# Performance work log

Hardware: AMD Instinct MI355X
Metric: run time of the kernel (lower is better)

## Reference

```python
import jax, jax.numpy as jnp
import numpy as np

N, D, OUT, K = 100000, 256, 128, 10
N1, B = 40960, 4096


def setup_inputs() -> dict:
    key = jax.random.key(0)
    k1, k2, k3, k4, k5, k6, k7 = jax.random.split(key, 7)
    raw_features = jax.random.normal(k1, (N, D), dtype=jnp.float32)
    # xavier-ish init for SageLayer weights [out, 2*in]
    W1 = jax.random.normal(k2, (OUT, 2 * D), dtype=jnp.float32) * (2.0 / (OUT + 2 * D)) ** 0.5
    W2 = jax.random.normal(k3, (OUT, 2 * OUT), dtype=jnp.float32) * (2.0 / (OUT + 2 * OUT)) ** 0.5
    nodes1 = jax.random.randint(k4, (N1,), 0, N)              # layer-1 node ids into raw table
    neighs1 = jax.random.randint(k5, (N1, K), 0, N)           # sampled neighbors (ids into raw table)
    map2 = jax.random.randint(k6, (B,), 0, N1)                # self-index of batch nodes into layer-1 rows
    neighs2 = jax.random.randint(k7, (B, K), 0, N1)           # sampled neighbors (rows of layer-1 embs)
    return {"raw_features": raw_features, "W1": W1, "W2": W2,
            "nodes1": nodes1, "neighs1": neighs1, "map2": map2, "neighs2": neighs2}


def reference(raw_features, W1, W2, nodes1, neighs1, map2, neighs2):
    # Layer 1: mean-aggregate sampled neighbor features (= mask.div(num_neigh).mm(embed_matrix))
    agg1 = jnp.mean(raw_features[neighs1], axis=1)                      # [N1, D]
    self1 = raw_features[nodes1]                                        # [N1, D]
    h1 = jax.nn.relu(jnp.concatenate([self1, agg1], axis=1) @ W1.T)     # [N1, OUT]
    # Layer 2
    agg2 = jnp.mean(h1[neighs2], axis=1)                                # [B, OUT]
    self2 = h1[map2]                                                    # [B, OUT]
    h2 = jax.nn.relu(jnp.concatenate([self2, agg2], axis=1) @ W2.T)     # [B, OUT]
    return h2
```

## Files before the change

### kernel.cpp

```cpp
#include <hip/hip_runtime.h>
#include <hip/hip_bf16.h>

#define N_RAW  100000
#define DIM    256
#define OUTD   128
#define KN     10
#define N1N    40960
#define BATCH  4096

typedef __attribute__((ext_vector_type(8))) short bf16x8;
typedef __attribute__((ext_vector_type(4))) float f32x4;
typedef unsigned int u32;

static __device__ inline float b2f(short s) {
  unsigned u = ((unsigned)(unsigned short)s) << 16;
  return __builtin_bit_cast(float, u);
}
static __device__ inline short f2b(float f) {
  unsigned u = __builtin_bit_cast(unsigned, f);
  unsigned r = (u + 0x7fff + ((u >> 16) & 1)) >> 16;
  return (short)r;
}

static __device__ inline void gload_lds16(const void* g, void* l) {
  __builtin_amdgcn_global_load_lds((const __attribute__((address_space(1))) u32*)g,
                                   (__attribute__((address_space(3))) u32*)l, 16, 0, 0);
}

__global__ void build_wc(const float* __restrict__ W1, const float* __restrict__ W2,
                         short* __restrict__ W1c, short* __restrict__ W2c) {
  int i = blockIdx.x * blockDim.x + threadIdx.x;
  {
    int j = i >> 8, k = i & 255;
    float v = (j < OUTD) ? W1[j * (2 * DIM) + k] : W1[(j - OUTD) * (2 * DIM) + DIM + k];
    u32 byte = (u32)(j * 512 + k * 2) ^ ((u32)(j & 7) << 4);
    *(short*)((char*)W1c + byte) = f2b(v);
  }
  if (i < 256 * 128) {
    int j = i >> 7, k = i & 127;
    float v = (j < OUTD) ? W2[j * (2 * OUTD) + k] : W2[(j - OUTD) * (2 * OUTD) + OUTD + k];
    u32 byte = (u32)(j * 256 + k * 2) ^ ((u32)(j & 7) << 4);
    *(short*)((char*)W2c + byte) = f2b(v);
  }
}

__launch_bounds__(512, 2)
__global__ void gemm_P(const float* __restrict__ raw, const short* __restrict__ W1c,
                       short* __restrict__ P) {
  __shared__ short Wlds[256 * 256];
  const int tid  = threadIdx.x;
  const int wave = tid >> 6, lane = tid & 63;
  const int r16  = lane & 15, kg = lane >> 4;
  const int m0   = blockIdx.x * 128 + wave * 16;

  int arow = m0 + r16; if (arow >= N_RAW) arow = N_RAW - 1;
  const float* xrow = raw + (size_t)arow * DIM + kg * 8;
  float4 af[16];
#pragma unroll
  for (int ks = 0; ks < 8; ++ks) {
    af[2 * ks]     = *(const float4*)(xrow + ks * 32);
    af[2 * ks + 1] = *(const float4*)(xrow + ks * 32 + 4);
  }

#pragma unroll
  for (int it = 0; it < 16; ++it)
    gload_lds16((const char*)W1c + it * 8192 + tid * 16,
                (char*)Wlds + it * 8192 + wave * 1024);
  __syncthreads();

  bf16x8 ab[8];
#pragma unroll
  for (int ks = 0; ks < 8; ++ks) {
    bf16x8 t;
    t[0] = f2b(af[2 * ks].x);     t[1] = f2b(af[2 * ks].y);
    t[2] = f2b(af[2 * ks].z);     t[3] = f2b(af[2 * ks].w);
    t[4] = f2b(af[2 * ks + 1].x); t[5] = f2b(af[2 * ks + 1].y);
    t[6] = f2b(af[2 * ks + 1].z); t[7] = f2b(af[2 * ks + 1].w);
    ab[ks] = t;
  }

  f32x4 acc[16];
#pragma unroll
  for (int n = 0; n < 16; ++n) acc[n] = (f32x4){0.f, 0.f, 0.f, 0.f};

#pragma unroll
  for (int ks = 0; ks < 8; ++ks) {
#pragma unroll
    for (int n = 0; n < 16; ++n) {
      u32 byte = (u32)((n * 16 + r16) * 512 + ks * 64 + kg * 16) ^ ((u32)(r16 & 7) << 4);
      bf16x8 b = *(const bf16x8*)((const char*)Wlds + byte);
      acc[n] = __builtin_amdgcn_mfma_f32_16x16x32_bf16(ab[ks], b, acc[n], 0, 0, 0);
    }
  }

#pragma unroll
  for (int n = 0; n < 16; ++n)
#pragma unroll
    for (int j = 0; j < 4; ++j) {
      int r = m0 + kg * 4 + j;
      if (r < N_RAW) P[(size_t)r * 256 + (n * 16 + r16)] = f2b(acc[n][j]);
    }
}

__launch_bounds__(512, 4)
__global__ void gemm_Q(const short* __restrict__ h1, const short* __restrict__ W2c,
                       short* __restrict__ Q) {
  __shared__ short Wlds[256 * 128];
  const int tid  = threadIdx.x;
  const int wave = tid >> 6, lane = tid & 63;
  const int r16  = lane & 15, kg = lane >> 4;
  const int m0   = blockIdx.x * 128 + wave * 16;

  const short* xrow = h1 + (size_t)(m0 + r16) * OUTD + kg * 8;
  bf16x8 ab[4];
#pragma unroll
  for (int ks = 0; ks < 4; ++ks) ab[ks] = *(const bf16x8*)(xrow + ks * 32);

#pragma unroll
  for (int it = 0; it < 8; ++it)
    gload_lds16((const char*)W2c + it * 8192 + tid * 16,
                (char*)Wlds + it * 8192 + wave * 1024);
  __syncthreads();

  f32x4 acc[16];
#pragma unroll
  for (int n = 0; n < 16; ++n) acc[n] = (f32x4){0.f, 0.f, 0.f, 0.f};

#pragma unroll
  for (int ks = 0; ks < 4; ++ks) {
#pragma unroll
    for (int n = 0; n < 16; ++n) {
      u32 byte = (u32)((n * 16 + r16) * 256 + ks * 64 + kg * 16) ^ ((u32)(r16 & 7) << 4);
      bf16x8 b = *(const bf16x8*)((const char*)Wlds + byte);
      acc[n] = __builtin_amdgcn_mfma_f32_16x16x32_bf16(ab[ks], b, acc[n], 0, 0, 0);
    }
  }

#pragma unroll
  for (int n = 0; n < 16; ++n)
#pragma unroll
    for (int j = 0; j < 4; ++j)
      Q[(size_t)(m0 + kg * 4 + j) * 256 + (n * 16 + r16)] = f2b(acc[n][j]);
}

__global__ void gather1(const short* __restrict__ P, const int* __restrict__ nodes1,
                        const int* __restrict__ neighs1, short* __restrict__ h1) {
  int g = threadIdx.x >> 4, t = threadIdx.x & 15;
  int row = blockIdx.x * 16 + g;
  int sn = nodes1[row];
  bf16x8 sv = *(const bf16x8*)(P + (size_t)sn * 256 + t * 8);
  float acc[8];
#pragma unroll
  for (int e = 0; e < 8; ++e) acc[e] = 0.f;
#pragma unroll
  for (int k = 0; k < KN; ++k) {
    int nn = neighs1[row * KN + k];
    bf16x8 nv = *(const bf16x8*)(P + (size_t)nn * 256 + 128 + t * 8);
#pragma unroll
    for (int e = 0; e < 8; ++e) acc[e] += b2f(nv[e]);
  }
  bf16x8 o;
#pragma unroll
  for (int e = 0; e < 8; ++e) o[e] = f2b(fmaxf(b2f(sv[e]) + 0.1f * acc[e], 0.f));
  *(bf16x8*)(h1 + (size_t)row * OUTD + t * 8) = o;
}

__global__ void gather2(const short* __restrict__ Q, const int* __restrict__ map2,
                        const int* __restrict__ neighs2, float* __restrict__ out) {
  int g = threadIdx.x >> 4, t = threadIdx.x & 15;
  int row = blockIdx.x * 16 + g;
  int sn = map2[row];
  bf16x8 sv = *(const bf16x8*)(Q + (size_t)sn * 256 + t * 8);
  float acc[8];
#pragma unroll
  for (int e = 0; e < 8; ++e) acc[e] = 0.f;
#pragma unroll
  for (int k = 0; k < KN; ++k) {
    int nn = neighs2[row * KN + k];
    bf16x8 nv = *(const bf16x8*)(Q + (size_t)nn * 256 + 128 + t * 8);
#pragma unroll
    for (int e = 0; e < 8; ++e) acc[e] += b2f(nv[e]);
  }
  float* orow = out + (size_t)row * OUTD + t * 8;
  float4 o0, o1;
  o0.x = fmaxf(b2f(sv[0]) + 0.1f * acc[0], 0.f);
  o0.y = fmaxf(b2f(sv[1]) + 0.1f * acc[1], 0.f);
  o0.z = fmaxf(b2f(sv[2]) + 0.1f * acc[2], 0.f);
  o0.w = fmaxf(b2f(sv[3]) + 0.1f * acc[3], 0.f);
  o1.x = fmaxf(b2f(sv[4]) + 0.1f * acc[4], 0.f);
  o1.y = fmaxf(b2f(sv[5]) + 0.1f * acc[5], 0.f);
  o1.z = fmaxf(b2f(sv[6]) + 0.1f * acc[6], 0.f);
  o1.w = fmaxf(b2f(sv[7]) + 0.1f * acc[7], 0.f);
  *(float4*)orow = o0;
  *(float4*)(orow + 4) = o1;
}

extern "C" void kernel_launch(void* const* d_in, const int* in_sizes, int n_in,
                              void* d_out, int out_size, void* d_ws, size_t ws_size,
                              hipStream_t stream) {
  const float* raw     = (const float*)d_in[0];
  const float* W1      = (const float*)d_in[1];
  const float* W2      = (const float*)d_in[2];
  const int*   nodes1  = (const int*)d_in[3];
  const int*   neighs1 = (const int*)d_in[4];
  const int*   map2    = (const int*)d_in[5];
  const int*   neighs2 = (const int*)d_in[6];
  float* out = (float*)d_out;

  char* ws = (char*)d_ws;
  short* W1c = (short*)(ws);
  short* W2c = (short*)(ws + 131072);
  short* P   = (short*)(ws + 196608);
  short* Q   = (short*)(ws + 196608);
  short* h1  = (short*)(ws + 51396608);

  build_wc<<<256, 256, 0, stream>>>(W1, W2, W1c, W2c);
  gemm_P<<<782, 512, 0, stream>>>(raw, W1c, P);
  gather1<<<N1N / 16, 256, 0, stream>>>(P, nodes1, neighs1, h1);
  gemm_Q<<<N1N / 128, 512, 0, stream>>>(h1, W2c, Q);
  gather2<<<BATCH / 16, 256, 0, stream>>>(Q, map2, neighs2, out);
}
```

Before: 93.22 us.

## Split GEMMs across output-column quarters to shrink LDS and raise occupancy

```diff
diff --git a/kernel.cpp b/kernel.cpp
--- a/kernel.cpp
+++ b/kernel.cpp
@@ -7,9 +7,12 @@
 #define KN     10
 #define N1N    40960
 #define BATCH  4096
+#define SNP    6250
+#define SNQ    2560
 
 typedef __attribute__((ext_vector_type(8))) short bf16x8;
 typedef __attribute__((ext_vector_type(4))) float f32x4;
+typedef __attribute__((ext_vector_type(4))) unsigned int u32x4;
 typedef unsigned int u32;
 
 static __device__ inline float b2f(short s) {
@@ -21,7 +24,11 @@
   unsigned r = (u + 0x7fff + ((u >> 16) & 1)) >> 16;
   return (short)r;
 }
-
+static __device__ inline u32 cvtpk(float lo, float hi) {
+  u32 r;
+  asm("v_cvt_pk_bf16_f32 %0, %1, %2" : "=v"(r) : "v"(lo), "v"(hi));
+  return r;
+}
 static __device__ inline void gload_lds16(const void* g, void* l) {
   __builtin_amdgcn_global_load_lds((const __attribute__((address_space(1))) u32*)g,
                                    (__attribute__((address_space(3))) u32*)l, 16, 0, 0);
@@ -33,114 +40,127 @@
   {
     int j = i >> 8, k = i & 255;
     float v = (j < OUTD) ? W1[j * (2 * DIM) + k] : W1[(j - OUTD) * (2 * DIM) + DIM + k];
-    u32 byte = (u32)(j * 512 + k * 2) ^ ((u32)(j & 7) << 4);
+    u32 byte = (u32)((j >> 6) * 32768 + (k >> 6) * 8192 + (j & 63) * 128)
+             + (((u32)(2 * (k & 63))) ^ ((u32)(j & 7) << 4));
     *(short*)((char*)W1c + byte) = f2b(v);
   }
   if (i < 256 * 128) {
     int j = i >> 7, k = i & 127;
     float v = (j < OUTD) ? W2[j * (2 * OUTD) + k] : W2[(j - OUTD) * (2 * OUTD) + OUTD + k];
-    u32 byte = (u32)(j * 256 + k * 2) ^ ((u32)(j & 7) << 4);
+    u32 byte = (u32)((j >> 6) * 16384 + (k >> 6) * 8192 + (j & 63) * 128)
+             + (((u32)(2 * (k & 63))) ^ ((u32)(j & 7) << 4));
     *(short*)((char*)W2c + byte) = f2b(v);
   }
 }
 
-__launch_bounds__(512, 2)
-__global__ void gemm_P(const float* __restrict__ raw, const short* __restrict__ W1c,
-                       short* __restrict__ P) {
-  __shared__ short Wlds[256 * 256];
+__global__ __launch_bounds__(512, 8)
+void gemm_P(const float* __restrict__ raw, const short* __restrict__ W1c,
+            short* __restrict__ P) {
+  __shared__ char Blds[32768];
   const int tid  = threadIdx.x;
   const int wave = tid >> 6, lane = tid & 63;
   const int r16  = lane & 15, kg = lane >> 4;
-  const int m0   = blockIdx.x * 128 + wave * 16;
-
-  int arow = m0 + r16; if (arow >= N_RAW) arow = N_RAW - 1;
-  const float* xrow = raw + (size_t)arow * DIM + kg * 8;
-  float4 af[16];
-#pragma unroll
-  for (int ks = 0; ks < 8; ++ks) {
-    af[2 * ks]     = *(const float4*)(xrow + ks * 32);
-    af[2 * ks + 1] = *(const float4*)(xrow + ks * 32 + 4);
-  }
-
-#pragma unroll
-  for (int it = 0; it < 16; ++it)
-    gload_lds16((const char*)W1c + it * 8192 + tid * 16,
-                (char*)Wlds + it * 8192 + wave * 1024);
+  const int q    = blockIdx.x & 3;
+  const int sg   = blockIdx.x >> 2;
+  const u32 swz  = (u32)(r16 & 7) << 4;
+
+#pragma unroll
+  for (int it = 0; it < 4; ++it)
+    gload_lds16((const char*)W1c + q * 32768 + it * 8192 + wave * 1024 + lane * 16,
+                Blds + it * 8192 + wave * 1024);
   __syncthreads();
 
-  bf16x8 ab[8];
-#pragma unroll
-  for (int ks = 0; ks < 8; ++ks) {
-    bf16x8 t;
-    t[0] = f2b(af[2 * ks].x);     t[1] = f2b(af[2 * ks].y);
-    t[2] = f2b(af[2 * ks].z);     t[3] = f2b(af[2 * ks].w);
-    t[4] = f2b(af[2 * ks + 1].x); t[5] = f2b(af[2 * ks + 1].y);
-    t[6] = f2b(af[2 * ks + 1].z); t[7] = f2b(af[2 * ks + 1].w);
-    ab[ks] = t;
-  }
-
-  f32x4 acc[16];
-#pragma unroll
-  for (int n = 0; n < 16; ++n) acc[n] = (f32x4){0.f, 0.f, 0.f, 0.f};
-
-#pragma unroll
-  for (int ks = 0; ks < 8; ++ks) {
-#pragma unroll
-    for (int n = 0; n < 16; ++n) {
-      u32 byte = (u32)((n * 16 + r16) * 512 + ks * 64 + kg * 16) ^ ((u32)(r16 & 7) << 4);
-      bf16x8 b = *(const bf16x8*)((const char*)Wlds + byte);
-      acc[n] = __builtin_amdgcn_mfma_f32_16x16x32_bf16(ab[ks], b, acc[n], 0, 0, 0);
+  const int s = sg * 8 + wave;
+  if (s >= SNP) return;
+
+  const float* x = raw + (size_t)(s * 16 + r16) * DIM + kg * 8;
+
+  f32x4 acc[4];
+#pragma unroll
+  for (int n = 0; n < 4; ++n) acc[n] = (f32x4){0.f, 0.f, 0.f, 0.f};
+
+#pragma unroll
+  for (int p = 0; p < 4; ++p) {
+    f32x4 v0 = *(const f32x4*)(x + p * 64);
+    f32x4 v1 = *(const f32x4*)(x + p * 64 + 4);
+    f32x4 v2 = *(const f32x4*)(x + p * 64 + 32);
+    f32x4 v3 = *(const f32x4*)(x + p * 64 + 36);
+
+    u32x4 t0, t1;
+    t0[0] = cvtpk(v0[0], v0[1]); t0[1] = cvtpk(v0[2], v0[3]);
+    t0[2] = cvtpk(v1[0], v1[1]); t0[3] = cvtpk(v1[2], v1[3]);
+    t1[0] = cvtpk(v2[0], v2[1]); t1[1] = cvtpk(v2[2], v2[3]);
+    t1[2] = cvtpk(v3[0], v3[1]); t1[3] = cvtpk(v3[2], v3[3]);
+    bf16x8 ab0 = __builtin_bit_cast(bf16x8, t0);
+    bf16x8 ab1 = __builtin_bit_cast(bf16x8, t1);
+
+#pragma unroll
+    for (int n = 0; n < 4; ++n) {
+      u32 base = (u32)(p * 8192 + (n * 16 + r16) * 128);
+      bf16x8 b0 = *(const bf16x8*)(Blds + base + (((u32)(kg * 16)) ^ swz));
+      bf16x8 b1 = *(const bf16x8*)(Blds + base + (((u32)(64 + kg * 16)) ^ swz));
+      acc[n] = __builtin_amdgcn_mfma_f32_16x16x32_bf16(ab0, b0, acc[n], 0, 0, 0);
+      acc[n] = __builtin_amdgcn_mfma_f32_16x16x32_bf16(ab1, b1, acc[n], 0, 0, 0);
     }
   }
 
-#pragma unroll
-  for (int n = 0; n < 16; ++n)
-#pragma unroll
-    for (int j = 0; j < 4; ++j) {
-      int r = m0 + kg * 4 + j;
-      if (r < N_RAW) P[(size_t)r * 256 + (n * 16 + r16)] = f2b(acc[n][j]);
-    }
-}
-
-__launch_bounds__(512, 4)
-__global__ void gemm_Q(const short* __restrict__ h1, const short* __restrict__ W2c,
-                       short* __restrict__ Q) {
-  __shared__ short Wlds[256 * 128];
+  short* pb = P + (size_t)(s * 16 + kg * 4) * 256 + q * 64 + r16;
+#pragma unroll
+  for (int n = 0; n < 4; ++n)
+#pragma unroll
+    for (int j = 0; j < 4; ++j)
+      pb[j * 256 + n * 16] = f2b(acc[n][j]);
+}
+
+__global__ __launch_bounds__(512, 8)
+void gemm_Q(const short* __restrict__ h1, const short* __restrict__ W2c,
+            short* __restrict__ Q) {
+  __shared__ char Blds[16384];
   const int tid  = threadIdx.x;
   const int wave = tid >> 6, lane = tid & 63;
   const int r16  = lane & 15, kg = lane >> 4;
-  const int m0   = blockIdx.x * 128 + wave * 16;
-
-  const short* xrow = h1 + (size_t)(m0 + r16) * OUTD + kg * 8;
-  bf16x8 ab[4];
-#pragma unroll
-  for (int ks = 0; ks < 4; ++ks) ab[ks] = *(const bf16x8*)(xrow + ks * 32);
-
-#pragma unroll
-  for (int it = 0; it < 8; ++it)
-    gload_lds16((const char*)W2c + it * 8192 + tid * 16,
-                (char*)Wlds + it * 8192 + wave * 1024);
+  const int q    = blockIdx.x & 3;
+  const int sg   = blockIdx.x >> 2;
+  const u32 swz  = (u32)(r16 & 7) << 4;
+
+#pragma unroll
+  for (int it = 0; it < 2; ++it)
+    gload_lds16((const char*)W2c + q * 16384 + it * 8192 + wave * 1024 + lane * 16,
+                Blds + it * 8192 + wave * 1024);
   __syncthreads();
 
-  f32x4 acc[16];
-#pragma unroll
-  for (int n = 0; n < 16; ++n) acc[n] = (f32x4){0.f, 0.f, 0.f, 0.f};
-
-#pragma unroll
-  for (int ks = 0; ks < 4; ++ks) {
-#pragma unroll
-    for (int n = 0; n < 16; ++n) {
-      u32 byte = (u32)((n * 16 + r16) * 256 + ks * 64 + kg * 16) ^ ((u32)(r16 & 7) << 4);
-      bf16x8 b = *(const bf16x8*)((const char*)Wlds + byte);
-      acc[n] = __builtin_amdgcn_mfma_f32_16x16x32_bf16(ab[ks], b, acc[n], 0, 0, 0);
-    }
-  }
-
-#pragma unroll
-  for (int n = 0; n < 16; ++n)
+  const int s = sg * 8 + wave;
+  if (s >= SNQ) return;
+
+  const short* x = h1 + (size_t)(s * 16 + r16) * OUTD + kg * 8;
+  bf16x8 a0 = *(const bf16x8*)(x);
+  bf16x8 a1 = *(const bf16x8*)(x + 32);
+  bf16x8 a2 = *(const bf16x8*)(x + 64);
+  bf16x8 a3 = *(const bf16x8*)(x + 96);
+
+  f32x4 acc[4];
+#pragma unroll
+  for (int n = 0; n < 4; ++n) acc[n] = (f32x4){0.f, 0.f, 0.f, 0.f};
+
+#pragma unroll
+  for (int n = 0; n < 4; ++n) {
+    u32 row = (u32)((n * 16 + r16) * 128);
+    bf16x8 b0 = *(const bf16x8*)(Blds + row + (((u32)(kg * 16)) ^ swz));
+    bf16x8 b1 = *(const bf16x8*)(Blds + row + (((u32)(64 + kg * 16)) ^ swz));
+    bf16x8 b2 = *(const bf16x8*)(Blds + 8192 + row + (((u32)(kg * 16)) ^ swz));
+    bf16x8 b3 = *(const bf16x8*)(Blds + 8192 + row + (((u32)(64 + kg * 16)) ^ swz));
+    acc[n] = __builtin_amdgcn_mfma_f32_16x16x32_bf16(a0, b0, acc[n], 0, 0, 0);
+    acc[n] = __builtin_amdgcn_mfma_f32_16x16x32_bf16(a1, b1, acc[n], 0, 0, 0);
+    acc[n] = __builtin_amdgcn_mfma_f32_16x16x32_bf16(a2, b2, acc[n], 0, 0, 0);
+    acc[n] = __builtin_amdgcn_mfma_f32_16x16x32_bf16(a3, b3, acc[n], 0, 0, 0);
+  }
+
+  short* qb = Q + (size_t)(s * 16 + kg * 4) * 256 + q * 64 + r16;
+#pragma unroll
+  for (int n = 0; n < 4; ++n)
 #pragma unroll
     for (int j = 0; j < 4; ++j)
-      Q[(size_t)(m0 + kg * 4 + j) * 256 + (n * 16 + r16)] = f2b(acc[n][j]);
+      qb[j * 256 + n * 16] = f2b(acc[n][j]);
 }
 
 __global__ void gather1(const short* __restrict__ P, const int* __restrict__ nodes1,
@@ -215,8 +235,8 @@
   short* h1  = (short*)(ws + 51396608);
 
   build_wc<<<256, 256, 0, stream>>>(W1, W2, W1c, W2c);
-  gemm_P<<<782, 512, 0, stream>>>(raw, W1c, P);
+  gemm_P<<<3128, 512, 0, stream>>>(raw, W1c, P);
   gather1<<<N1N / 16, 256, 0, stream>>>(P, nodes1, neighs1, h1);
-  gemm_Q<<<N1N / 128, 512, 0, stream>>>(h1, W2c, Q);
+  gemm_Q<<<1280, 512, 0, stream>>>(h1, W2c, Q);
   gather2<<<BATCH / 16, 256, 0, stream>>>(Q, map2, neighs2, out);
 }
```

After: 112.9 us. 1.21x slower.
